# Kernel tuning notes

Hardware: AMD Instinct MI355X
Metric: run time of the kernel (lower is better)

## Reference

```python
import jax, jax.numpy as jnp
import numpy as np
from jax import lax

B, IN_C, OUT_C, Z_DIM, H, W = 16, 128, 128, 128, 64, 64
K, NUM_GROUPS, EPS = 3, 8, 1e-5


def setup_inputs() -> dict:
    key = jax.random.key(0)
    ks = jax.random.split(key, 10)
    s = 1.0 / np.sqrt(Z_DIM)
    return {
        "x": jax.random.normal(ks[0], (B, IN_C, H, W), dtype=jnp.float32),
        "z": jax.random.normal(ks[1], (B, Z_DIM), dtype=jnp.float32),
        # hypernet head for conv1: z_dim -> out_c*in_c*k*k
        "h1_w": jax.random.normal(ks[2], (Z_DIM, OUT_C * IN_C * K * K), dtype=jnp.float32) * s,
        "h1_b": jax.random.normal(ks[3], (OUT_C * IN_C * K * K,), dtype=jnp.float32) * 0.01,
        # hypernet head for conv2: z_dim -> out_c*out_c*k*k
        "h2_w": jax.random.normal(ks[4], (Z_DIM, OUT_C * OUT_C * K * K), dtype=jnp.float32) * s,
        "h2_b": jax.random.normal(ks[5], (OUT_C * OUT_C * K * K,), dtype=jnp.float32) * 0.01,
        "gamma1": jnp.ones((OUT_C,), dtype=jnp.float32),
        "beta1": jnp.zeros((OUT_C,), dtype=jnp.float32),
        "gamma2": jnp.ones((OUT_C,), dtype=jnp.float32),
        "beta2": jnp.zeros((OUT_C,), dtype=jnp.float32),
    }


def _per_sample_conv(x, w, stride, pad):
    # x: [B,C,H,W], w: [B,O,I,k,k] -> [B,O,H',W'] (per-sample weights)
    def one(xi, wi):
        return lax.conv_general_dilated(
            xi[None], wi, (stride, stride), [(pad, pad), (pad, pad)],
            dimension_numbers=("NCHW", "OIHW", "NCHW"))[0]
    return jax.vmap(one)(x, w)


def _group_norm(x, gamma, beta):
    b, c, h, w = x.shape
    xg = x.reshape(b, NUM_GROUPS, -1)
    mean = xg.mean(axis=-1, keepdims=True)
    var = xg.var(axis=-1, keepdims=True)
    xg = (xg - mean) * lax.rsqrt(var + EPS)
    x = xg.reshape(b, c, h, w)
    return x * gamma[None, :, None, None] + beta[None, :, None, None]


def reference(x, z, h1_w, h1_b, h2_w, h2_b, gamma1, beta1, gamma2, beta2):
    w1 = (z @ h1_w + h1_b).reshape(B, OUT_C, IN_C, K, K)
    out = _per_sample_conv(x, w1, 1, K // 2)
    out = jax.nn.relu(_group_norm(out, gamma1, beta1))
    w2 = (z @ h2_w + h2_b).reshape(B, OUT_C, OUT_C, K, K)
    out = _per_sample_conv(out, w2, 1, K // 2)
    out = _group_norm(out, gamma2, beta2)
    return jax.nn.relu(out + x)  # identity shortcut (stride=1, in_c==out_c)
```

## Files before the change

kernel.cpp:

```cpp
#include <hip/hip_runtime.h>

#define BB 16
#define CC 128
#define HH 64
#define WW 64
#define NG 8
#define WPB 147456
#define PLANE 4096
#define GROUP_N 65536.f

typedef __attribute__((ext_vector_type(8))) short short8;
typedef __attribute__((ext_vector_type(4))) float floatx4;
typedef __attribute__((ext_vector_type(4))) unsigned short ushortx4;

__device__ __forceinline__ unsigned short f2bf(float f) {
    unsigned u = __builtin_bit_cast(unsigned, f);
    return (unsigned short)((u + 0x7fffu + ((u >> 16) & 1u)) >> 16);
}
__device__ __forceinline__ float bf2f(unsigned short h) {
    unsigned u = ((unsigned)h) << 16;
    return __builtin_bit_cast(float, u);
}

__global__ __launch_bounds__(256)
void transpose_in(const float* __restrict__ x, unsigned short* __restrict__ xt)
{
    int blk = blockIdx.x;
    int b = blk >> 8, icc = (blk >> 6) & 3, y = blk & 63;
    int xi = threadIdx.x & 63, vg = threadIdx.x >> 6;
    const float* src = x + (((size_t)(b * CC + icc * 32 + vg * 8)) * HH + y) * WW + xi;
    short8 o;
#pragma unroll
    for (int e = 0; e < 8; ++e) o[e] = (short)f2bf(src[(size_t)e * PLANE]);
    unsigned short* dst = xt + (((size_t)(b * 4 + icc) * PLANE) + y * WW + xi) * 32 + vg * 8;
    *(short8*)dst = o;
}

__global__ __launch_bounds__(256)
void stream_gemm(const float* __restrict__ z,
                 const float* __restrict__ h1w, const float* __restrict__ h1b,
                 const float* __restrict__ h2w, const float* __restrict__ h2b,
                 unsigned short* __restrict__ P)
{
    const int blk = blockIdx.x;
    const int which = (blk >= 576) ? 1 : 0;
    const int n = (blk - which * 576) * 256 + threadIdx.x;
    const float* __restrict__ hw = which ? h2w : h1w;
    const float* __restrict__ hb = which ? h2b : h1b;
    unsigned short* pw = P + (size_t)which * 2359296;

    float acc[BB];
#pragma unroll
    for (int b = 0; b < BB; ++b) acc[b] = 0.f;

    for (int k0 = 0; k0 < 128; k0 += 8) {
        float hv[8];
#pragma unroll
        for (int u = 0; u < 8; ++u) hv[u] = hw[(size_t)(k0 + u) * WPB + n];
#pragma unroll
        for (int u = 0; u < 8; ++u) {
#pragma unroll
            for (int b = 0; b < BB; ++b)
                acc[b] = fmaf(z[b * 128 + k0 + u], hv[u], acc[b]);
        }
    }
    const float bias = hb[n];
#pragma unroll
    for (int b = 0; b < BB; ++b)
        pw[(size_t)b * WPB + n] = f2bf(acc[b] + bias);
}

__global__ __launch_bounds__(256)
void repack(const unsigned short* __restrict__ P,
            unsigned short* __restrict__ wf1, unsigned short* __restrict__ wf2)
{
    int gid = blockIdx.x * 256 + threadIdx.x;
    int which = gid >> 15, g = gid & 32767;
    int lane = g & 63, frag = (g >> 6) & 7, icc = (g >> 9) & 3, b = g >> 11;

    const unsigned short* src = P + (size_t)which * 2359296 + (size_t)b * WPB
        + (frag * 16 + (lane & 15)) * 1152 + (icc * 32 + (lane >> 4) * 8) * 9;
    unsigned short buf[72];
#pragma unroll
    for (int i = 0; i < 9; ++i)
        *(short8*)(buf + i * 8) = *(const short8*)(src + i * 8);

    unsigned short* wf = which ? wf2 : wf1;
#pragma unroll
    for (int tap = 0; tap < 9; ++tap) {
        short8 o;
#pragma unroll
        for (int j = 0; j < 8; ++j) o[j] = (short)buf[j * 9 + tap];
        size_t off = ((((size_t)(b * 4 + icc) * 9 + tap) * 8 + frag) * 64 + lane) * 8;
        *(short8*)(wf + off) = o;
    }
}

template <int MODE>
__global__ __launch_bounds__(256, 2)
void conv_mfma(const unsigned short* __restrict__ xt,
               const unsigned short* __restrict__ wf,
               unsigned short* __restrict__ yt, float* __restrict__ ynchw,
               float* __restrict__ stats)
{
    const int blk = blockIdx.x;
    const int b = blk >> 5, tile = blk & 31;
    const int tid = threadIdx.x;
    const int w = tid >> 6, lane = tid & 63;
    const int i = w >> 1, j = w & 1;
    const int q = lane >> 4, n16 = lane & 15;
    const int y = tile * 2 + j;

    floatx4 acc[4][4];
#pragma unroll
    for (int mf = 0; mf < 4; ++mf)
#pragma unroll
        for (int nf = 0; nf < 4; ++nf) acc[mf][nf] = (floatx4)0.f;

    const unsigned short* xtb_b = xt + (size_t)b * 4 * PLANE * 32;
    const unsigned short* wf_b  = wf + (size_t)b * WPB;

    for (int icc = 0; icc < 4; ++icc) {
        const unsigned short* xtb = xtb_b + (size_t)icc * PLANE * 32;
        const unsigned short* wfc = wf_b + (size_t)icc * 36864;
#pragma unroll
        for (int tap = 0; tap < 9; ++tap) {
            const int dy = tap / 3 - 1, dx = tap % 3 - 1;
            const int yy = y + dy;
            if ((unsigned)yy >= (unsigned)HH) continue;

            short8 a[4], bbf[4];
#pragma unroll
            for (int mf = 0; mf < 4; ++mf)
                a[mf] = *(const short8*)(wfc + (((size_t)(tap * 8 + i * 4 + mf)) * 64 + lane) * 8);
#pragma unroll
            for (int nf = 0; nf < 4; ++nf) {
                int xx = nf * 16 + n16 + dx;
                if ((unsigned)xx < (unsigned)WW)
                    bbf[nf] = *(const short8*)(xtb + ((size_t)(yy * WW + xx)) * 32 + q * 8);
                else
                    bbf[nf] = (short8)0;
            }
#pragma unroll
            for (int mf = 0; mf < 4; ++mf)
#pragma unroll
                for (int nf = 0; nf < 4; ++nf)
                    acc[mf][nf] = __builtin_amdgcn_mfma_f32_16x16x32_bf16(
                        a[mf], bbf[nf], acc[mf][nf], 0, 0, 0);
        }
    }

#pragma unroll
    for (int mf = 0; mf < 4; ++mf) {
        float s1 = 0.f, s2 = 0.f;
#pragma unroll
        for (int nf = 0; nf < 4; ++nf) {
#pragma unroll
            for (int r = 0; r < 4; ++r) {
                float v = acc[mf][nf][r];
                s1 += v; s2 += v * v;
            }
            const int xx = nf * 16 + n16;
            if (MODE == 0) {
                const int icc1 = i * 2 + (mf >> 1);
                const int v0 = (mf & 1) * 16 + q * 4;
                unsigned short* p = yt + (((size_t)(b * 4 + icc1) * PLANE) + y * WW + xx) * 32 + v0;
                ushortx4 u;
                u.x = f2bf(acc[mf][nf][0]); u.y = f2bf(acc[mf][nf][1]);
                u.z = f2bf(acc[mf][nf][2]); u.w = f2bf(acc[mf][nf][3]);
                *(ushortx4*)p = u;
            } else {
#pragma unroll
                for (int r = 0; r < 4; ++r) {
                    int oc = i * 64 + mf * 16 + q * 4 + r;
                    ynchw[(((size_t)(b * CC + oc)) * HH + y) * WW + xx] = acc[mf][nf][r];
                }
            }
        }
#pragma unroll
        for (int off = 32; off > 0; off >>= 1) {
            s1 += __shfl_down(s1, off, 64);
            s2 += __shfl_down(s2, off, 64);
        }
        if (lane == 0) {
            int g = i * 4 + mf;
            atomicAdd(&stats[(b * NG + g) * 2 + 0], s1);
            atomicAdd(&stats[(b * NG + g) * 2 + 1], s2);
        }
    }
}

__global__ __launch_bounds__(256)
void norm_relu_bf16(unsigned short* __restrict__ yt, const float* __restrict__ stats,
                    const float* __restrict__ gamma, const float* __restrict__ beta)
{
    int idx8 = blockIdx.x * 256 + threadIdx.x;
    int t = idx8 >> 2;
    int bicc = t >> 12;
    int b = bicc >> 2, icc = bicc & 3;
    int cb = icc * 32 + (idx8 & 3) * 8;
    int g = cb >> 4;
    float sum = stats[(b * NG + g) * 2 + 0];
    float ssq = stats[(b * NG + g) * 2 + 1];
    float mean = sum * (1.f / GROUP_N);
    float var  = ssq * (1.f / GROUP_N) - mean * mean;
    float inv  = rsqrtf(var + 1e-5f);

    short8 d = *(short8*)(yt + (size_t)idx8 * 8);
    short8 o;
#pragma unroll
    for (int e = 0; e < 8; ++e) {
        float s = gamma[cb + e] * inv;
        float tt = beta[cb + e] - mean * s;
        float v = bf2f((unsigned short)d[e]);
        o[e] = (short)f2bf(fmaxf(v * s + tt, 0.f));
    }
    *(short8*)(yt + (size_t)idx8 * 8) = o;
}

__global__ __launch_bounds__(256)
void gn_add_relu(float* __restrict__ y2, const float* __restrict__ x,
                 const float* __restrict__ stats, const float* __restrict__ gamma,
                 const float* __restrict__ beta)
{
    const int bc = blockIdx.x;
    const int b = bc >> 7, c = bc & 127;
    const int g = c >> 4;
    float sum  = stats[(b * NG + g) * 2 + 0];
    float ssq  = stats[(b * NG + g) * 2 + 1];
    float mean = sum * (1.f / GROUP_N);
    float var  = ssq * (1.f / GROUP_N) - mean * mean;
    float inv  = rsqrtf(var + 1e-5f);
    float s = gamma[c] * inv;
    float t = beta[c] - mean * s;

    size_t base = (size_t)bc * PLANE;
    float4* yp = (float4*)(y2 + base);
    const float4* xp = (const float4*)(x + base);
    for (int i = threadIdx.x; i < PLANE / 4; i += 256) {
        float4 v = yp[i], xv = xp[i];
        v.x = fmaxf(v.x * s + t + xv.x, 0.f);
        v.y = fmaxf(v.y * s + t + xv.y, 0.f);
        v.z = fmaxf(v.z * s + t + xv.z, 0.f);
        v.w = fmaxf(v.w * s + t + xv.w, 0.f);
        yp[i] = v;
    }
}

extern "C" void kernel_launch(void* const* d_in, const int* in_sizes, int n_in,
                              void* d_out, int out_size, void* d_ws, size_t ws_size,
                              hipStream_t stream)
{
    const float* x   = (const float*)d_in[0];
    const float* z   = (const float*)d_in[1];
    const float* h1w = (const float*)d_in[2];
    const float* h1b = (const float*)d_in[3];
    const float* h2w = (const float*)d_in[4];
    const float* h2b = (const float*)d_in[5];
    const float* g1  = (const float*)d_in[6];
    const float* b1  = (const float*)d_in[7];
    const float* g2  = (const float*)d_in[8];
    const float* b2  = (const float*)d_in[9];
    float* out = (float*)d_out;

    float* stats1 = (float*)d_ws;
    float* stats2 = stats1 + 256;
    unsigned short* wf1 = (unsigned short*)((char*)d_ws + 2048);
    unsigned short* wf2 = wf1 + 2359296;
    unsigned short* xt0 = wf2 + 2359296;
    unsigned short* xt1 = xt0 + 8388608;
    unsigned short* P   = xt1;

    hipMemsetAsync(d_ws, 0, 2048, stream);

    transpose_in<<<4096, 256, 0, stream>>>(x, xt0);

    stream_gemm<<<1152, 256, 0, stream>>>(z, h1w, h1b, h2w, h2b, P);
    repack<<<256, 256, 0, stream>>>(P, wf1, wf2);

    conv_mfma<0><<<512, 256, 0, stream>>>(xt0, wf1, xt1, nullptr, stats1);

    norm_relu_bf16<<<4096, 256, 0, stream>>>(xt1, stats1, g1, b1);

    conv_mfma<1><<<512, 256, 0, stream>>>(xt1, wf2, nullptr, out, stats2);

    gn_add_relu<<<2048, 256, 0, stream>>>(out, x, stats2, g2, b2);
}
```

Baseline: 373.9 us.

## Merge hypernet GEMM and input transpose into one launch, vectorize GEMM, drop memset

```diff
diff --git a/kernel.cpp b/kernel.cpp
--- a/kernel.cpp
+++ b/kernel.cpp
@@ -23,57 +23,84 @@
 }
 
 __global__ __launch_bounds__(256)
-void transpose_in(const float* __restrict__ x, unsigned short* __restrict__ xt)
-{
-    int blk = blockIdx.x;
-    int b = blk >> 8, icc = (blk >> 6) & 3, y = blk & 63;
-    int xi = threadIdx.x & 63, vg = threadIdx.x >> 6;
-    const float* src = x + (((size_t)(b * CC + icc * 32 + vg * 8)) * HH + y) * WW + xi;
-    short8 o;
-#pragma unroll
-    for (int e = 0; e < 8; ++e) o[e] = (short)f2bf(src[(size_t)e * PLANE]);
-    unsigned short* dst = xt + (((size_t)(b * 4 + icc) * PLANE) + y * WW + xi) * 32 + vg * 8;
-    *(short8*)dst = o;
-}
-
-__global__ __launch_bounds__(256)
-void stream_gemm(const float* __restrict__ z,
-                 const float* __restrict__ h1w, const float* __restrict__ h1b,
-                 const float* __restrict__ h2w, const float* __restrict__ h2b,
-                 unsigned short* __restrict__ P)
-{
-    const int blk = blockIdx.x;
-    const int which = (blk >= 576) ? 1 : 0;
-    const int n = (blk - which * 576) * 256 + threadIdx.x;
-    const float* __restrict__ hw = which ? h2w : h1w;
-    const float* __restrict__ hb = which ? h2b : h1b;
-    unsigned short* pw = P + (size_t)which * 2359296;
-
-    float acc[BB];
-#pragma unroll
-    for (int b = 0; b < BB; ++b) acc[b] = 0.f;
-
-    for (int k0 = 0; k0 < 128; k0 += 8) {
-        float hv[8];
-#pragma unroll
-        for (int u = 0; u < 8; ++u) hv[u] = hw[(size_t)(k0 + u) * WPB + n];
-#pragma unroll
-        for (int u = 0; u < 8; ++u) {
-#pragma unroll
-            for (int b = 0; b < BB; ++b)
-                acc[b] = fmaf(z[b * 128 + k0 + u], hv[u], acc[b]);
-        }
-    }
-    const float bias = hb[n];
-#pragma unroll
-    for (int b = 0; b < BB; ++b)
-        pw[(size_t)b * WPB + n] = f2bf(acc[b] + bias);
+void prep(const float* __restrict__ x, const float* __restrict__ z,
+          const float* __restrict__ h1w, const float* __restrict__ h1b,
+          const float* __restrict__ h2w, const float* __restrict__ h2b,
+          unsigned short* __restrict__ xt, unsigned short* __restrict__ P)
+{
+    __shared__ float zs[2048];
+    const int tid = threadIdx.x;
+
+    if (blockIdx.x < 288) {
+        for (int i = tid; i < 2048; i += 256) zs[i] = z[i];
+        __syncthreads();
+
+        const int gwin  = blockIdx.x * 4 + (tid >> 6);
+        const int which = (gwin >= 576) ? 1 : 0;
+        const int win   = gwin - which * 576;
+        const float* __restrict__ hw = which ? h2w : h1w;
+        const float* __restrict__ hb = which ? h2b : h1b;
+        const int n = win * 256 + (tid & 63) * 4;
+
+        float acc[16][4];
+#pragma unroll
+        for (int b = 0; b < 16; ++b)
+#pragma unroll
+            for (int c = 0; c < 4; ++c) acc[b][c] = 0.f;
+
+        for (int k0 = 0; k0 < 128; k0 += 8) {
+            float4 hv[8];
+#pragma unroll
+            for (int u = 0; u < 8; ++u)
+                hv[u] = *(const float4*)(hw + (size_t)(k0 + u) * WPB + n);
+#pragma unroll
+            for (int b = 0; b < 16; ++b) {
+                const float* zp = &zs[b * 128 + k0];
+#pragma unroll
+                for (int u = 0; u < 8; ++u) {
+                    float zv = zp[u];
+                    acc[b][0] = fmaf(zv, hv[u].x, acc[b][0]);
+                    acc[b][1] = fmaf(zv, hv[u].y, acc[b][1]);
+                    acc[b][2] = fmaf(zv, hv[u].z, acc[b][2]);
+                    acc[b][3] = fmaf(zv, hv[u].w, acc[b][3]);
+                }
+            }
+        }
+
+        const float4 bias = *(const float4*)(hb + n);
+        unsigned short* pw = P + (size_t)which * 2359296;
+#pragma unroll
+        for (int b = 0; b < 16; ++b) {
+            ushortx4 u4;
+            u4.x = f2bf(acc[b][0] + bias.x);
+            u4.y = f2bf(acc[b][1] + bias.y);
+            u4.z = f2bf(acc[b][2] + bias.z);
+            u4.w = f2bf(acc[b][3] + bias.w);
+            *(ushortx4*)(pw + (size_t)b * WPB + n) = u4;
+        }
+    } else {
+        int blk = blockIdx.x - 288;
+        int b = blk >> 8, icc = (blk >> 6) & 3, y = blk & 63;
+        int xi = tid & 63, vg = tid >> 6;
+        const float* src = x + (((size_t)(b * CC + icc * 32 + vg * 8)) * HH + y) * WW + xi;
+        short8 o;
+#pragma unroll
+        for (int e = 0; e < 8; ++e) o[e] = (short)f2bf(src[(size_t)e * PLANE]);
+        unsigned short* dst = xt + (((size_t)(b * 4 + icc) * PLANE) + y * WW + xi) * 32 + vg * 8;
+        *(short8*)dst = o;
+    }
 }
 
 __global__ __launch_bounds__(256)
 void repack(const unsigned short* __restrict__ P,
-            unsigned short* __restrict__ wf1, unsigned short* __restrict__ wf2)
-{
+            unsigned short* __restrict__ wf1, unsigned short* __restrict__ wf2,
+            float* __restrict__ stats)
+{
+    if (blockIdx.x == 0) {
+        stats[threadIdx.x] = 0.f;
+        stats[threadIdx.x + 256] = 0.f;
+    }
+
     int gid = blockIdx.x * 256 + threadIdx.x;
     int which = gid >> 15, g = gid & 32767;
     int lane = g & 63, frag = (g >> 6) & 7, icc = (g >> 9) & 3, b = g >> 11;
@@ -271,12 +298,9 @@
     unsigned short* xt1 = xt0 + 8388608;
     unsigned short* P   = xt1;
 
-    hipMemsetAsync(d_ws, 0, 2048, stream);
-
-    transpose_in<<<4096, 256, 0, stream>>>(x, xt0);
-
-    stream_gemm<<<1152, 256, 0, stream>>>(z, h1w, h1b, h2w, h2b, P);
-    repack<<<256, 256, 0, stream>>>(P, wf1, wf2);
+    prep<<<288 + 4096, 256, 0, stream>>>(x, z, h1w, h1b, h2w, h2b, xt0, P);
+
+    repack<<<256, 256, 0, stream>>>(P, wf1, wf2, stats1);
 
     conv_mfma<0><<<512, 256, 0, stream>>>(xt0, wf1, xt1, nullptr, stats1);
 
```

Measured after the change: 374.4 us. No clear change (+0.1%).

## Fuse independent stages into shared launches to overlap hypernet GEMMs with conv

Applied to the files above, without the earlier changes.

```diff
diff --git a/kernel.cpp b/kernel.cpp
--- a/kernel.cpp
+++ b/kernel.cpp
@@ -22,33 +22,14 @@
     return __builtin_bit_cast(float, u);
 }
 
-__global__ __launch_bounds__(256)
-void transpose_in(const float* __restrict__ x, unsigned short* __restrict__ xt)
-{
-    int blk = blockIdx.x;
-    int b = blk >> 8, icc = (blk >> 6) & 3, y = blk & 63;
-    int xi = threadIdx.x & 63, vg = threadIdx.x >> 6;
-    const float* src = x + (((size_t)(b * CC + icc * 32 + vg * 8)) * HH + y) * WW + xi;
-    short8 o;
-#pragma unroll
-    for (int e = 0; e < 8; ++e) o[e] = (short)f2bf(src[(size_t)e * PLANE]);
-    unsigned short* dst = xt + (((size_t)(b * 4 + icc) * PLANE) + y * WW + xi) * 32 + vg * 8;
-    *(short8*)dst = o;
-}
-
-__global__ __launch_bounds__(256)
-void stream_gemm(const float* __restrict__ z,
-                 const float* __restrict__ h1w, const float* __restrict__ h1b,
-                 const float* __restrict__ h2w, const float* __restrict__ h2b,
-                 unsigned short* __restrict__ P)
-{
-    const int blk = blockIdx.x;
-    const int which = (blk >= 576) ? 1 : 0;
-    const int n = (blk - which * 576) * 256 + threadIdx.x;
-    const float* __restrict__ hw = which ? h2w : h1w;
-    const float* __restrict__ hb = which ? h2b : h1b;
-    unsigned short* pw = P + (size_t)which * 2359296;
-
+
+__device__ __forceinline__ void gemm_head(int gblk, int tid,
+                                          const float* __restrict__ z,
+                                          const float* __restrict__ hw,
+                                          const float* __restrict__ hb,
+                                          unsigned short* __restrict__ pw)
+{
+    const int n = gblk * 256 + tid;
     float acc[BB];
 #pragma unroll
     for (int b = 0; b < BB; ++b) acc[b] = 0.f;
@@ -70,22 +51,17 @@
         pw[(size_t)b * WPB + n] = f2bf(acc[b] + bias);
 }
 
-__global__ __launch_bounds__(256)
-void repack(const unsigned short* __restrict__ P,
-            unsigned short* __restrict__ wf1, unsigned short* __restrict__ wf2)
-{
-    int gid = blockIdx.x * 256 + threadIdx.x;
-    int which = gid >> 15, g = gid & 32767;
-    int lane = g & 63, frag = (g >> 6) & 7, icc = (g >> 9) & 3, b = g >> 11;
-
-    const unsigned short* src = P + (size_t)which * 2359296 + (size_t)b * WPB
+__device__ __forceinline__ void repack_head(int gid,
+                                            const unsigned short* __restrict__ P,
+                                            unsigned short* __restrict__ wf)
+{
+    int lane = gid & 63, frag = (gid >> 6) & 7, icc = (gid >> 9) & 3, b = gid >> 11;
+    const unsigned short* src = P + (size_t)b * WPB
         + (frag * 16 + (lane & 15)) * 1152 + (icc * 32 + (lane >> 4) * 8) * 9;
     unsigned short buf[72];
 #pragma unroll
     for (int i = 0; i < 9; ++i)
         *(short8*)(buf + i * 8) = *(const short8*)(src + i * 8);
-
-    unsigned short* wf = which ? wf2 : wf1;
 #pragma unroll
     for (int tap = 0; tap < 9; ++tap) {
         short8 o;
@@ -97,15 +73,14 @@
 }
 
 template <int MODE>
-__global__ __launch_bounds__(256, 2)
-void conv_mfma(const unsigned short* __restrict__ xt,
-               const unsigned short* __restrict__ wf,
-               unsigned short* __restrict__ yt, float* __restrict__ ynchw,
-               float* __restrict__ stats)
-{
-    const int blk = blockIdx.x;
+__device__ __forceinline__ void conv_body(int blk, int tid,
+                                          const unsigned short* __restrict__ xt,
+                                          const unsigned short* __restrict__ wf,
+                                          unsigned short* __restrict__ yt,
+                                          float* __restrict__ ynchw,
+                                          float* __restrict__ stats)
+{
     const int b = blk >> 5, tile = blk & 31;
-    const int tid = threadIdx.x;
     const int w = tid >> 6, lane = tid & 63;
     const int i = w >> 1, j = w & 1;
     const int q = lane >> 4, n16 = lane & 15;
@@ -191,10 +166,61 @@
 }
 
 __global__ __launch_bounds__(256)
-void norm_relu_bf16(unsigned short* __restrict__ yt, const float* __restrict__ stats,
-                    const float* __restrict__ gamma, const float* __restrict__ beta)
-{
-    int idx8 = blockIdx.x * 256 + threadIdx.x;
+void gemm1_transpose(const float* __restrict__ x, const float* __restrict__ z,
+                     const float* __restrict__ h1w, const float* __restrict__ h1b,
+                     unsigned short* __restrict__ xt, unsigned short* __restrict__ P1)
+{
+    const int tid = threadIdx.x;
+    if (blockIdx.x < 576) {
+        gemm_head(blockIdx.x, tid, z, h1w, h1b, P1);
+    } else {
+        int blk = blockIdx.x - 576;
+        int b = blk >> 8, icc = (blk >> 6) & 3, y = blk & 63;
+        int xi = tid & 63, vg = tid >> 6;
+        const float* src = x + (((size_t)(b * CC + icc * 32 + vg * 8)) * HH + y) * WW + xi;
+        short8 o;
+#pragma unroll
+        for (int e = 0; e < 8; ++e) o[e] = (short)f2bf(src[(size_t)e * PLANE]);
+        unsigned short* dst = xt + (((size_t)(b * 4 + icc) * PLANE) + y * WW + xi) * 32 + vg * 8;
+        *(short8*)dst = o;
+    }
+}
+
+__global__ __launch_bounds__(256)
+void repack1(const unsigned short* __restrict__ P1, unsigned short* __restrict__ wf1,
+             float* __restrict__ stats)
+{
+    if (blockIdx.x == 0) {
+        stats[threadIdx.x] = 0.f;
+        stats[threadIdx.x + 256] = 0.f;
+    }
+    repack_head(blockIdx.x * 256 + threadIdx.x, P1, wf1);
+}
+
+__global__ __launch_bounds__(256, 2)
+void conv1_gemm2(const unsigned short* __restrict__ xt0,
+                 const unsigned short* __restrict__ wf1,
+                 unsigned short* __restrict__ xt1, float* __restrict__ stats1,
+                 const float* __restrict__ z,
+                 const float* __restrict__ h2w, const float* __restrict__ h2b,
+                 unsigned short* __restrict__ P2)
+{
+    if (blockIdx.x < 512)
+        conv_body<0>(blockIdx.x, threadIdx.x, xt0, wf1, xt1, nullptr, stats1);
+    else
+        gemm_head(blockIdx.x - 512, threadIdx.x, z, h2w, h2b, P2);
+}
+
+__global__ __launch_bounds__(256)
+void repack2_norm(const unsigned short* __restrict__ P2, unsigned short* __restrict__ wf2,
+                  unsigned short* __restrict__ yt, const float* __restrict__ stats,
+                  const float* __restrict__ gamma, const float* __restrict__ beta)
+{
+    if (blockIdx.x < 128) {
+        repack_head(blockIdx.x * 256 + threadIdx.x, P2, wf2);
+        return;
+    }
+    int idx8 = (blockIdx.x - 128) * 256 + threadIdx.x;
     int t = idx8 >> 2;
     int bicc = t >> 12;
     int b = bicc >> 2, icc = bicc & 3;
@@ -216,6 +242,14 @@
         o[e] = (short)f2bf(fmaxf(v * s + tt, 0.f));
     }
     *(short8*)(yt + (size_t)idx8 * 8) = o;
+}
+
+__global__ __launch_bounds__(256, 2)
+void conv2(const unsigned short* __restrict__ xt1,
+           const unsigned short* __restrict__ wf2,
+           float* __restrict__ out, float* __restrict__ stats2)
+{
+    conv_body<1>(blockIdx.x, threadIdx.x, xt1, wf2, nullptr, out, stats2);
 }
 
 __global__ __launch_bounds__(256)
@@ -269,20 +303,19 @@
     unsigned short* wf2 = wf1 + 2359296;
     unsigned short* xt0 = wf2 + 2359296;
     unsigned short* xt1 = xt0 + 8388608;
-    unsigned short* P   = xt1;
-
-    hipMemsetAsync(d_ws, 0, 2048, stream);
-
-    transpose_in<<<4096, 256, 0, stream>>>(x, xt0);
-
-    stream_gemm<<<1152, 256, 0, stream>>>(z, h1w, h1b, h2w, h2b, P);
-    repack<<<256, 256, 0, stream>>>(P, wf1, wf2);
-
-    conv_mfma<0><<<512, 256, 0, stream>>>(xt0, wf1, xt1, nullptr, stats1);
-
-    norm_relu_bf16<<<4096, 256, 0, stream>>>(xt1, stats1, g1, b1);
-
-    conv_mfma<1><<<512, 256, 0, stream>>>(xt1, wf2, nullptr, out, stats2);
+    unsigned short* P1  = xt1;
+    unsigned short* P2  = (unsigned short*)d_out;
+
+    gemm1_transpose<<<576 + 4096, 256, 0, stream>>>(x, z, h1w, h1b, xt0, P1);
+
+    repack1<<<128, 256, 0, stream>>>(P1, wf1, stats1);
+
+    conv1_gemm2<<<512 + 576, 256, 0, stream>>>(xt0, wf1, xt1, stats1,
+                                               z, h2w, h2b, P2);
+
+    repack2_norm<<<128 + 4096, 256, 0, stream>>>(P2, wf2, xt1, stats1, g1, b1);
+
+    conv2<<<512, 256, 0, stream>>>(xt1, wf2, out, stats2);
 
     gn_add_relu<<<2048, 256, 0, stream>>>(out, x, stats2, g2, b2);
 }
```

Measured after the change: 379.9 us. About the same (+1.6%).
